# Kernel tuning notes

Measured on AMD Instinct MI355X. Metric: run time of the kernel, lower is better.

## Reference

```python
import jax, jax.numpy as jnp
import numpy as np

TAU = 2.0          # LIF membrane time constant
VTH = 1.0          # spike threshold
ALPHA = 2.0        # ATan surrogate default alpha
EPS = 1e-5         # LayerNorm eps


@jax.custom_vjp
def atan_spike(x):
    # Heaviside forward, ATan surrogate gradient backward (spikingjelly surrogate.ATan)
    return (x >= 0.0).astype(x.dtype)

def _spike_fwd(x):
    return atan_spike(x), x

def _spike_bwd(x, g):
    sg = (ALPHA / 2.0) / (1.0 + (jnp.pi / 2.0 * ALPHA * x) ** 2)
    return (g * sg,)

atan_spike.defvjp(_spike_fwd, _spike_bwd)


def lif_scan(xs):
    # xs: [T, B, C]; multi-step LIF with decay_input=True, v_reset=0.0 (hard reset),
    # detach_reset=True (reset path is stop_gradient'ed).
    def step(v, x):
        h = v + (x - v) / TAU                      # charge
        s = atan_spike(h - VTH)                    # fire
        v_new = h * (1.0 - jax.lax.stop_gradient(s))  # hard reset to 0, detached
        return v_new, s
    _, spikes = jax.lax.scan(step, jnp.zeros_like(xs[0]), xs)
    return spikes


def setup_inputs() -> dict:
    key = jax.random.key(0)
    ks = jax.random.split(key, 5)
    B, T, D, H = 32, 2048, 128, 256
    x = jax.random.normal(ks[0], (B, T, D), dtype=jnp.float32)
    W1 = jax.random.normal(ks[1], (H, D), dtype=jnp.float32) * (1.0 / np.sqrt(D))
    b1 = jax.random.normal(ks[2], (H,), dtype=jnp.float32) * 0.02
    W2 = jax.random.normal(ks[3], (D, H), dtype=jnp.float32) * (1.0 / np.sqrt(H))
    b2 = jax.random.normal(ks[4], (D,), dtype=jnp.float32) * 0.02
    ln_w = jnp.ones((D,), dtype=jnp.float32)
    ln_b = jnp.zeros((D,), dtype=jnp.float32)
    return {"x": x, "W1": W1, "b1": b1, "W2": W2, "b2": b2, "ln_w": ln_w, "ln_b": ln_b}


def reference(x, W1, b1, W2, b2, ln_w, ln_b):
    # x: [B, T, D] -> time-major [T, B, D]
    h = jnp.swapaxes(x, 0, 1)
    h = h @ W1.T + b1            # [T, B, H]
    h = lif_scan(h)              # spikes in {0,1}
    h = h @ W2.T + b2            # [T, B, D]
    h = lif_scan(h)
    h = jnp.swapaxes(h, 0, 1)    # back to [B, T, D]
    y = x + h                    # residual
    mu = jnp.mean(y, axis=-1, keepdims=True)
    var = jnp.mean((y - mu) ** 2, axis=-1, keepdims=True)
    return (y - mu) * jax.lax.rsqrt(var + EPS) * ln_w + ln_b
```

## Files before the change

### kernel.cpp

```cpp
#include <hip/hip_runtime.h>


typedef _Float16 half8 __attribute__((ext_vector_type(8)));
typedef float f32x4 __attribute__((ext_vector_type(4)));

#define MFMA_F16(a, b, c) __builtin_amdgcn_mfma_f32_16x16x32_f16(a, b, c, 0, 0, 0)

__device__ __forceinline__ unsigned short h2u(_Float16 h) {
    union { _Float16 h; unsigned short u; } x; x.h = h; return x.u;
}

__device__ __forceinline__ void split8(float4 f0, float4 f1, half8& a, half8& b) {
    float fs[8] = {f0.x, f0.y, f0.z, f0.w, f1.x, f1.y, f1.z, f1.w};
    half8 ha, hb;
#pragma unroll
    for (int q = 0; q < 8; ++q) {
        ha[q] = (_Float16)fs[q];
        hb[q] = (_Float16)(fs[q] - (float)ha[q]);
    }
    a = ha; b = hb;
}

__global__ __launch_bounds__(512, 1) void mega_kernel(
    const float* __restrict__ X,
    const float* __restrict__ W1, const float* __restrict__ W2,
    const float* __restrict__ b1, const float* __restrict__ b2,
    const float* __restrict__ lnw, const float* __restrict__ lnb,
    float* __restrict__ out)
{
    __shared__ __align__(16) float h1T[256 * 36];
    __shared__ __align__(16) float h2T[128 * 36];
    __shared__ __align__(16) float s2buf[2][32 * 132];
    __shared__ __align__(16) unsigned short spkbuf[32 * 264];
    __shared__ __align__(16) unsigned short xb[2][32 * 136];

    const int tid = threadIdx.x;
    const int lane = tid & 63;
    const int w = tid >> 6;
    const bool isS = (tid < 256);
    const int sg = w;
    const int gg = w - 4;
    const int fr = lane & 15;
    const int fo8 = (lane >> 4) * 8;
    const int qr = (lane >> 4) * 4;
    const int b = blockIdx.y;
    const int t0 = blockIdx.x * 256;
    const int s0 = (blockIdx.x == 0) ? 4 : 0;

    const float* __restrict__ xbase = X + (size_t)b * 2048 * 128;
    float* __restrict__ obase = out + (size_t)b * 2048 * 128;

    half8 wf[32];
    float bias0[4];
    if (isS) {
#pragma unroll
        for (int j = 0; j < 2; ++j) {
            const size_t d = (size_t)(32 * sg + 16 * j + fr) * 256;
#pragma unroll
            for (int ks = 0; ks < 8; ++ks) {
                float4 f0 = *(const float4*)&W2[d + ks * 32 + fo8];
                float4 f1 = *(const float4*)&W2[d + ks * 32 + fo8 + 4];
                split8(f0, f1, wf[(j * 8 + ks) * 2], wf[(j * 8 + ks) * 2 + 1]);
            }
            bias0[j] = b2[32 * sg + 16 * j + fr];
        }
    } else {
#pragma unroll
        for (int j = 0; j < 4; ++j) {
            const size_t n = (size_t)(64 * gg + 16 * j + fr) * 128;
#pragma unroll
            for (int k0 = 0; k0 < 4; ++k0) {
                float4 f0 = *(const float4*)&W1[n + k0 * 32 + fo8];
                float4 f1 = *(const float4*)&W1[n + k0 * 32 + fo8 + 4];
                split8(f0, f1, wf[(j * 4 + k0) * 2], wf[(j * 4 + k0) * 2 + 1]);
            }
            bias0[j] = b1[64 * gg + 16 * j + fr];
        }
    }
    const float2 wv = *(const float2*)(lnw + lane * 2);
    const float2 bbv = *(const float2*)(lnb + lane * 2);

    float v1 = 0.0f, v2 = 0.0f;
    const int d2 = (tid - 256) & 127;
    const int tgs = (tid - 384) & 127;
    const int srow = tgs >> 5;
    const int sc4 = (tgs & 31) * 4;
    float4 pfx[8];
    float2 pflnC[4], pflnN[4];

    if (tid >= 384) {
        const int tb = t0 - 128 + s0 * 32;
#pragma unroll
        for (int q = 0; q < 8; ++q) {
            float4 xv = *(const float4*)&xbase[(size_t)(tb + srow + 4 * q) * 128 + sc4];
            _Float16 a0 = (_Float16)xv.x, e0 = (_Float16)(xv.x - (float)a0);
            _Float16 a1 = (_Float16)xv.y, e1 = (_Float16)(xv.y - (float)a1);
            _Float16 a2 = (_Float16)xv.z, e2 = (_Float16)(xv.z - (float)a2);
            _Float16 a3 = (_Float16)xv.w, e3 = (_Float16)(xv.w - (float)a3);
            ushort4 ua = {h2u(a0), h2u(a1), h2u(a2), h2u(a3)};
            ushort4 ue = {h2u(e0), h2u(e1), h2u(e2), h2u(e3)};
            *(ushort4*)&xb[0][(srow + 4 * q) * 136 + sc4] = ua;
            *(ushort4*)&xb[1][(srow + 4 * q) * 136 + sc4] = ue;
        }
    }
    __syncthreads();
    if (!isS) {
        const _Float16* xa0 = (const _Float16*)&xb[0][0];
        const _Float16* xa1 = (const _Float16*)&xb[1][0];
#pragma unroll
        for (int h = 0; h < 2; ++h) {
            f32x4 acc[4];
#pragma unroll
            for (int j = 0; j < 4; ++j) acc[j] = (f32x4){0.f, 0.f, 0.f, 0.f};
#pragma unroll
            for (int k0 = 0; k0 < 4; ++k0) {
                half8 a0 = *(const half8*)&xa0[(fr + 16 * h) * 136 + k0 * 32 + fo8];
                half8 a1 = *(const half8*)&xa1[(fr + 16 * h) * 136 + k0 * 32 + fo8];
#pragma unroll
                for (int j = 0; j < 4; ++j) {
                    acc[j] = MFMA_F16(a0, wf[(j * 4 + k0) * 2], acc[j]);
                    acc[j] = MFMA_F16(a0, wf[(j * 4 + k0) * 2 + 1], acc[j]);
                    acc[j] = MFMA_F16(a1, wf[(j * 4 + k0) * 2], acc[j]);
                }
            }
#pragma unroll
            for (int j = 0; j < 4; ++j) {
                int col = 64 * gg + 16 * j + fr;
                float4 o;
                o.x = acc[j][0] + bias0[j];
                o.y = acc[j][1] + bias0[j];
                o.z = acc[j][2] + bias0[j];
                o.w = acc[j][3] + bias0[j];
                *(float4*)&h1T[col * 36 + qr + 16 * h] = o;
            }
        }
        if (tid >= 384) {
            const int tb = t0 - 128 + s0 * 32 + 32;
#pragma unroll
            for (int q = 0; q < 8; ++q)
                pfx[q] = *(const float4*)&xbase[(size_t)(tb + srow + 4 * q) * 128 + sc4];
        }
    }
    __syncthreads();

    for (int sc = s0; sc <= 13; ++sc) {
        const int tbase = t0 - 128 + sc * 32;

        if (sc >= 6) {
            const int tbm = tbase - 64;
            const float* s2r = &s2buf[sc & 1][0];
#pragma unroll
            for (int rr = 0; rr < 4; ++rr) {
                int row = 4 * w + rr;
                float2 s2v = *(const float2*)&s2r[row * 132 + lane * 2];
                float y0 = pflnC[rr].x + s2v.x;
                float y1 = pflnC[rr].y + s2v.y;
                float sum = y0 + y1;
                float ss = y0 * y0 + y1 * y1;
#pragma unroll
                for (int off = 32; off > 0; off >>= 1) {
                    sum += __shfl_xor(sum, off, 64);
                    ss  += __shfl_xor(ss, off, 64);
                }
                float mu = sum * (1.0f / 128.0f);
                float var = ss * (1.0f / 128.0f) - mu * mu;
                float inv = rsqrtf(var + 1e-5f);
                float2 o;
                o.x = (y0 - mu) * inv * wv.x + bbv.x;
                o.y = (y1 - mu) * inv * wv.y + bbv.y;
                *(float2*)&obase[(size_t)(tbm + row) * 128 + lane * 2] = o;
            }
        }
        if (isS) {
            if (sc <= 11) {
                float4 hv[8];
#pragma unroll
                for (int k = 0; k < 8; ++k)
                    hv[k] = *(const float4*)&h1T[tid * 36 + 4 * k];
                __builtin_amdgcn_s_setprio(1);
#pragma unroll
                for (int t = 0; t < 32; ++t) {
                    float hh = (t & 3) == 0 ? hv[t >> 2].x
                             : (t & 3) == 1 ? hv[t >> 2].y
                             : (t & 3) == 2 ? hv[t >> 2].z : hv[t >> 2].w;
                    float h = v1 + (hh - v1) * 0.5f;
                    bool sp = (h >= 1.0f);
                    v1 = sp ? 0.0f : h;
                    spkbuf[t * 264 + tid] = sp ? (unsigned short)0x3C00 : (unsigned short)0;
                }
                __builtin_amdgcn_s_setprio(0);
            }
        } else if (tid < 384) {
            if (sc > s0 && sc <= 12) {
                float* s2w = &s2buf[(sc - 1) & 1][0];
                float4 hv[8];
#pragma unroll
                for (int k = 0; k < 8; ++k)
                    hv[k] = *(const float4*)&h2T[d2 * 36 + 4 * k];
                __builtin_amdgcn_s_setprio(1);
#pragma unroll
                for (int t = 0; t < 32; ++t) {
                    float hh = (t & 3) == 0 ? hv[t >> 2].x
                             : (t & 3) == 1 ? hv[t >> 2].y
                             : (t & 3) == 2 ? hv[t >> 2].z : hv[t >> 2].w;
                    float h = v2 + (hh - v2) * 0.5f;
                    bool sp = (h >= 1.0f);
                    v2 = sp ? 0.0f : h;
                    s2w[t * 132 + d2] = sp ? 1.0f : 0.0f;
                }
                __builtin_amdgcn_s_setprio(0);
            }
        } else {
            if (sc <= 10) {
#pragma unroll
                for (int q = 0; q < 8; ++q) {
                    float4 xv = pfx[q];
                    _Float16 a0 = (_Float16)xv.x, e0 = (_Float16)(xv.x - (float)a0);
                    _Float16 a1 = (_Float16)xv.y, e1 = (_Float16)(xv.y - (float)a1);
                    _Float16 a2 = (_Float16)xv.z, e2 = (_Float16)(xv.z - (float)a2);
                    _Float16 a3 = (_Float16)xv.w, e3 = (_Float16)(xv.w - (float)a3);
                    ushort4 ua = {h2u(a0), h2u(a1), h2u(a2), h2u(a3)};
                    ushort4 ue = {h2u(e0), h2u(e1), h2u(e2), h2u(e3)};
                    *(ushort4*)&xb[0][(srow + 4 * q) * 136 + sc4] = ua;
                    *(ushort4*)&xb[1][(srow + 4 * q) * 136 + sc4] = ue;
                }
            }
        }
        __syncthreads();

        if (sc >= 5 && sc <= 12) {
#pragma unroll
            for (int rr = 0; rr < 4; ++rr)
                pflnN[rr] = *(const float2*)&xbase[(size_t)(tbase - 32 + 4 * w + rr) * 128 + lane * 2];
        }
        if (isS) {
            if (sc <= 11) {
                const _Float16* sp = (const _Float16*)&spkbuf[0];
#pragma unroll
                for (int h = 0; h < 2; ++h) {
                    f32x4 acc[2];
                    acc[0] = (f32x4){0.f, 0.f, 0.f, 0.f};
                    acc[1] = (f32x4){0.f, 0.f, 0.f, 0.f};
#pragma unroll
                    for (int ks = 0; ks < 8; ++ks) {
                        half8 a = *(const half8*)&sp[(fr + 16 * h) * 264 + ks * 32 + fo8];
#pragma unroll
                        for (int j = 0; j < 2; ++j) {
                            acc[j] = MFMA_F16(a, wf[(j * 8 + ks) * 2], acc[j]);
                            acc[j] = MFMA_F16(a, wf[(j * 8 + ks) * 2 + 1], acc[j]);
                        }
                    }
#pragma unroll
                    for (int j = 0; j < 2; ++j) {
                        int col = 32 * sg + 16 * j + fr;
                        float4 o;
                        o.x = acc[j][0] + bias0[j];
                        o.y = acc[j][1] + bias0[j];
                        o.z = acc[j][2] + bias0[j];
                        o.w = acc[j][3] + bias0[j];
                        *(float4*)&h2T[col * 36 + qr + 16 * h] = o;
                    }
                }
            }
        } else {
            if (tid >= 384 && sc <= 9) {
#pragma unroll
                for (int q = 0; q < 8; ++q)
                    pfx[q] = *(const float4*)&xbase[(size_t)(tbase + 64 + srow + 4 * q) * 128 + sc4];
            }
            if (sc <= 10) {
                const _Float16* xa0 = (const _Float16*)&xb[0][0];
                const _Float16* xa1 = (const _Float16*)&xb[1][0];
#pragma unroll
                for (int h = 0; h < 2; ++h) {
                    f32x4 acc[4];
#pragma unroll
                    for (int j = 0; j < 4; ++j) acc[j] = (f32x4){0.f, 0.f, 0.f, 0.f};
#pragma unroll
                    for (int k0 = 0; k0 < 4; ++k0) {
                        half8 a0 = *(const half8*)&xa0[(fr + 16 * h) * 136 + k0 * 32 + fo8];
                        half8 a1 = *(const half8*)&xa1[(fr + 16 * h) * 136 + k0 * 32 + fo8];
#pragma unroll
                        for (int j = 0; j < 4; ++j) {
                            acc[j] = MFMA_F16(a0, wf[(j * 4 + k0) * 2], acc[j]);
                            acc[j] = MFMA_F16(a0, wf[(j * 4 + k0) * 2 + 1], acc[j]);
                            acc[j] = MFMA_F16(a1, wf[(j * 4 + k0) * 2], acc[j]);
                        }
                    }
#pragma unroll
                    for (int j = 0; j < 4; ++j) {
                        int col = 64 * gg + 16 * j + fr;
                        float4 o;
                        o.x = acc[j][0] + bias0[j];
                        o.y = acc[j][1] + bias0[j];
                        o.z = acc[j][2] + bias0[j];
                        o.w = acc[j][3] + bias0[j];
                        *(float4*)&h1T[col * 36 + qr + 16 * h] = o;
                    }
                }
            }
        }
#pragma unroll
        for (int rr = 0; rr < 4; ++rr) pflnC[rr] = pflnN[rr];
        __syncthreads();
    }
}

extern "C" void kernel_launch(void* const* d_in, const int* in_sizes, int n_in,
                              void* d_out, int out_size, void* d_ws, size_t ws_size,
                              hipStream_t stream)
{
    const float* x   = (const float*)d_in[0];
    const float* W1  = (const float*)d_in[1];
    const float* b1  = (const float*)d_in[2];
    const float* W2  = (const float*)d_in[3];
    const float* b2  = (const float*)d_in[4];
    const float* lnw = (const float*)d_in[5];
    const float* lnb = (const float*)d_in[6];
    float* out = (float*)d_out;

    dim3 gM(8, 32);
    mega_kernel<<<gM, 512, 0, stream>>>(x, W1, W2, b1, b2, lnw, lnb, out);
}
```

Baseline: 135.3 us.

## Double block to 1024 threads, splitting MFMA GEMM work across more waves

```diff
diff --git a/kernel.cpp b/kernel.cpp
--- a/kernel.cpp
+++ b/kernel.cpp
@@ -21,7 +21,7 @@
     a = ha; b = hb;
 }
 
-__global__ __launch_bounds__(512, 1) void mega_kernel(
+__global__ __launch_bounds__(1024, 4) void mega_kernel(
     const float* __restrict__ X,
     const float* __restrict__ W1, const float* __restrict__ W2,
     const float* __restrict__ b1, const float* __restrict__ b2,
@@ -37,9 +37,8 @@
     const int tid = threadIdx.x;
     const int lane = tid & 63;
     const int w = tid >> 6;
-    const bool isS = (tid < 256);
-    const int sg = w;
-    const int gg = w - 4;
+    const bool isS = (w < 8);
+    const int gG = w - 8;
     const int fr = lane & 15;
     const int fo8 = (lane >> 4) * 8;
     const int qr = (lane >> 4) * 4;
@@ -50,31 +49,28 @@
     const float* __restrict__ xbase = X + (size_t)b * 2048 * 128;
     float* __restrict__ obase = out + (size_t)b * 2048 * 128;
 
-    half8 wf[32];
-    float bias0[4];
+    half8 wf[16];
+    float bias0[2];
     if (isS) {
+        const size_t d = (size_t)(16 * w + fr) * 256;
+#pragma unroll
+        for (int ks = 0; ks < 8; ++ks) {
+            float4 f0 = *(const float4*)&W2[d + ks * 32 + fo8];
+            float4 f1 = *(const float4*)&W2[d + ks * 32 + fo8 + 4];
+            split8(f0, f1, wf[ks * 2], wf[ks * 2 + 1]);
+        }
+        bias0[0] = b2[16 * w + fr];
+    } else {
 #pragma unroll
         for (int j = 0; j < 2; ++j) {
-            const size_t d = (size_t)(32 * sg + 16 * j + fr) * 256;
-#pragma unroll
-            for (int ks = 0; ks < 8; ++ks) {
-                float4 f0 = *(const float4*)&W2[d + ks * 32 + fo8];
-                float4 f1 = *(const float4*)&W2[d + ks * 32 + fo8 + 4];
-                split8(f0, f1, wf[(j * 8 + ks) * 2], wf[(j * 8 + ks) * 2 + 1]);
-            }
-            bias0[j] = b2[32 * sg + 16 * j + fr];
-        }
-    } else {
-#pragma unroll
-        for (int j = 0; j < 4; ++j) {
-            const size_t n = (size_t)(64 * gg + 16 * j + fr) * 128;
+            const size_t n = (size_t)(32 * gG + 16 * j + fr) * 128;
 #pragma unroll
             for (int k0 = 0; k0 < 4; ++k0) {
                 float4 f0 = *(const float4*)&W1[n + k0 * 32 + fo8];
                 float4 f1 = *(const float4*)&W1[n + k0 * 32 + fo8 + 4];
                 split8(f0, f1, wf[(j * 4 + k0) * 2], wf[(j * 4 + k0) * 2 + 1]);
             }
-            bias0[j] = b1[64 * gg + 16 * j + fr];
+            bias0[j] = b1[32 * gG + 16 * j + fr];
         }
     }
     const float2 wv = *(const float2*)(lnw + lane * 2);
@@ -85,10 +81,11 @@
     const int tgs = (tid - 384) & 127;
     const int srow = tgs >> 5;
     const int sc4 = (tgs & 31) * 4;
+    const bool isStage = (tid >= 384 && tid < 512);
     float4 pfx[8];
-    float2 pflnC[4], pflnN[4];
-
-    if (tid >= 384) {
+    float2 pflnC[2], pflnN[2];
+
+    if (isStage) {
         const int tb = t0 - 128 + s0 * 32;
 #pragma unroll
         for (int q = 0; q < 8; ++q) {
@@ -109,23 +106,23 @@
         const _Float16* xa1 = (const _Float16*)&xb[1][0];
 #pragma unroll
         for (int h = 0; h < 2; ++h) {
-            f32x4 acc[4];
-#pragma unroll
-            for (int j = 0; j < 4; ++j) acc[j] = (f32x4){0.f, 0.f, 0.f, 0.f};
+            f32x4 acc[2];
+            acc[0] = (f32x4){0.f, 0.f, 0.f, 0.f};
+            acc[1] = (f32x4){0.f, 0.f, 0.f, 0.f};
 #pragma unroll
             for (int k0 = 0; k0 < 4; ++k0) {
                 half8 a0 = *(const half8*)&xa0[(fr + 16 * h) * 136 + k0 * 32 + fo8];
                 half8 a1 = *(const half8*)&xa1[(fr + 16 * h) * 136 + k0 * 32 + fo8];
 #pragma unroll
-                for (int j = 0; j < 4; ++j) {
+                for (int j = 0; j < 2; ++j) {
                     acc[j] = MFMA_F16(a0, wf[(j * 4 + k0) * 2], acc[j]);
                     acc[j] = MFMA_F16(a0, wf[(j * 4 + k0) * 2 + 1], acc[j]);
                     acc[j] = MFMA_F16(a1, wf[(j * 4 + k0) * 2], acc[j]);
                 }
             }
 #pragma unroll
-            for (int j = 0; j < 4; ++j) {
-                int col = 64 * gg + 16 * j + fr;
+            for (int j = 0; j < 2; ++j) {
+                int col = 32 * gG + 16 * j + fr;
                 float4 o;
                 o.x = acc[j][0] + bias0[j];
                 o.y = acc[j][1] + bias0[j];
@@ -134,12 +131,12 @@
                 *(float4*)&h1T[col * 36 + qr + 16 * h] = o;
             }
         }
-        if (tid >= 384) {
-            const int tb = t0 - 128 + s0 * 32 + 32;
-#pragma unroll
-            for (int q = 0; q < 8; ++q)
-                pfx[q] = *(const float4*)&xbase[(size_t)(tb + srow + 4 * q) * 128 + sc4];
-        }
+    }
+    if (isStage) {
+        const int tb = t0 - 128 + s0 * 32 + 32;
+#pragma unroll
+        for (int q = 0; q < 8; ++q)
+            pfx[q] = *(const float4*)&xbase[(size_t)(tb + srow + 4 * q) * 128 + sc4];
     }
     __syncthreads();
 
@@ -150,8 +147,8 @@
             const int tbm = tbase - 64;
             const float* s2r = &s2buf[sc & 1][0];
 #pragma unroll
-            for (int rr = 0; rr < 4; ++rr) {
-                int row = 4 * w + rr;
+            for (int rr = 0; rr < 2; ++rr) {
+                int row = 2 * w + rr;
                 float2 s2v = *(const float2*)&s2r[row * 132 + lane * 2];
                 float y0 = pflnC[rr].x + s2v.x;
                 float y1 = pflnC[rr].y + s2v.y;
@@ -171,7 +168,7 @@
                 *(float2*)&obase[(size_t)(tbm + row) * 128 + lane * 2] = o;
             }
         }
-        if (isS) {
+        if (tid < 256) {
             if (sc <= 11) {
                 float4 hv[8];
 #pragma unroll
@@ -210,7 +207,7 @@
                 }
                 __builtin_amdgcn_s_setprio(0);
             }
-        } else {
+        } else if (tid < 512) {
             if (sc <= 10) {
 #pragma unroll
                 for (int q = 0; q < 8; ++q) {
@@ -230,66 +227,58 @@
 
         if (sc >= 5 && sc <= 12) {
 #pragma unroll
-            for (int rr = 0; rr < 4; ++rr)
-                pflnN[rr] = *(const float2*)&xbase[(size_t)(tbase - 32 + 4 * w + rr) * 128 + lane * 2];
+            for (int rr = 0; rr < 2; ++rr)
+                pflnN[rr] = *(const float2*)&xbase[(size_t)(tbase - 32 + 2 * w + rr) * 128 + lane * 2];
+        }
+        if (isStage && sc <= 9) {
+#pragma unroll
+            for (int q = 0; q < 8; ++q)
+                pfx[q] = *(const float4*)&xbase[(size_t)(tbase + 64 + srow + 4 * q) * 128 + sc4];
         }
         if (isS) {
             if (sc <= 11) {
                 const _Float16* sp = (const _Float16*)&spkbuf[0];
+#pragma unroll
+                for (int h = 0; h < 2; ++h) {
+                    f32x4 acc = (f32x4){0.f, 0.f, 0.f, 0.f};
+#pragma unroll
+                    for (int ks = 0; ks < 8; ++ks) {
+                        half8 a = *(const half8*)&sp[(fr + 16 * h) * 264 + ks * 32 + fo8];
+                        acc = MFMA_F16(a, wf[ks * 2], acc);
+                        acc = MFMA_F16(a, wf[ks * 2 + 1], acc);
+                    }
+                    int col = 16 * w + fr;
+                    float4 o;
+                    o.x = acc[0] + bias0[0];
+                    o.y = acc[1] + bias0[0];
+                    o.z = acc[2] + bias0[0];
+                    o.w = acc[3] + bias0[0];
+                    *(float4*)&h2T[col * 36 + qr + 16 * h] = o;
+                }
+            }
+        } else {
+            if (sc <= 10) {
+                const _Float16* xa0 = (const _Float16*)&xb[0][0];
+                const _Float16* xa1 = (const _Float16*)&xb[1][0];
 #pragma unroll
                 for (int h = 0; h < 2; ++h) {
                     f32x4 acc[2];
                     acc[0] = (f32x4){0.f, 0.f, 0.f, 0.f};
                     acc[1] = (f32x4){0.f, 0.f, 0.f, 0.f};
 #pragma unroll
-                    for (int ks = 0; ks < 8; ++ks) {
-                        half8 a = *(const half8*)&sp[(fr + 16 * h) * 264 + ks * 32 + fo8];
-#pragma unroll
-                        for (int j = 0; j < 2; ++j) {
-                            acc[j] = MFMA_F16(a, wf[(j * 8 + ks) * 2], acc[j]);
-                            acc[j] = MFMA_F16(a, wf[(j * 8 + ks) * 2 + 1], acc[j]);
-                        }
-                    }
-#pragma unroll
-                    for (int j = 0; j < 2; ++j) {
-                        int col = 32 * sg + 16 * j + fr;
-                        float4 o;
-                        o.x = acc[j][0] + bias0[j];
-                        o.y = acc[j][1] + bias0[j];
-                        o.z = acc[j][2] + bias0[j];
-                        o.w = acc[j][3] + bias0[j];
-                        *(float4*)&h2T[col * 36 + qr + 16 * h] = o;
-                    }
-                }
-            }
-        } else {
-            if (tid >= 384 && sc <= 9) {
-#pragma unroll
-                for (int q = 0; q < 8; ++q)
-                    pfx[q] = *(const float4*)&xbase[(size_t)(tbase + 64 + srow + 4 * q) * 128 + sc4];
-            }
-            if (sc <= 10) {
-                const _Float16* xa0 = (const _Float16*)&xb[0][0];
-                const _Float16* xa1 = (const _Float16*)&xb[1][0];
-#pragma unroll
-                for (int h = 0; h < 2; ++h) {
-                    f32x4 acc[4];
-#pragma unroll
-                    for (int j = 0; j < 4; ++j) acc[j] = (f32x4){0.f, 0.f, 0.f, 0.f};
-#pragma unroll
                     for (int k0 = 0; k0 < 4; ++k0) {
                         half8 a0 = *(const half8*)&xa0[(fr + 16 * h) * 136 + k0 * 32 + fo8];
                         half8 a1 = *(const half8*)&xa1[(fr + 16 * h) * 136 + k0 * 32 + fo8];
 #pragma unroll
-                        for (int j = 0; j < 4; ++j) {
+                        for (int j = 0; j < 2; ++j) {
                             acc[j] = MFMA_F16(a0, wf[(j * 4 + k0) * 2], acc[j]);
                             acc[j] = MFMA_F16(a0, wf[(j * 4 + k0) * 2 + 1], acc[j]);
                             acc[j] = MFMA_F16(a1, wf[(j * 4 + k0) * 2], acc[j]);
                         }
                     }
 #pragma unroll
-                    for (int j = 0; j < 4; ++j) {
-                        int col = 64 * gg + 16 * j + fr;
+                    for (int j = 0; j < 2; ++j) {
+                        int col = 32 * gG + 16 * j + fr;
                         float4 o;
                         o.x = acc[j][0] + bias0[j];
                         o.y = acc[j][1] + bias0[j];
@@ -301,7 +290,7 @@
             }
         }
 #pragma unroll
-        for (int rr = 0; rr < 4; ++rr) pflnC[rr] = pflnN[rr];
+        for (int rr = 0; rr < 2; ++rr) pflnC[rr] = pflnN[rr];
         __syncthreads();
     }
 }
@@ -320,5 +309,5 @@
     float* out = (float*)d_out;
 
     dim3 gM(8, 32);
-    mega_kernel<<<gM, 512, 0, stream>>>(x, W1, W2, b1, b2, lnw, lnb, out);
+    mega_kernel<<<gM, 1024, 0, stream>>>(x, W1, W2, b1, b2, lnw, lnb, out);
 }
```

Result: slower. 295.8 us (+118.7%).
